# Kernel tuning notes

Hardware: AMD Instinct MI355X
Metric: run time of the kernel (lower is better)

Reference implementation:

```python
import jax, jax.numpy as jnp
import numpy as np

B, L, H, E, R = 2, 512, 768, 512, 32768
H2 = H // 2


def setup_inputs() -> dict:
    key = jax.random.key(0)
    ks = jax.random.split(key, 16)
    s = 0.02
    inp = {
        "hidden_states": jax.random.normal(ks[0], (B, L, H), dtype=jnp.float32),
        "ent_start": jax.random.randint(ks[1], (B, E), 0, L, dtype=jnp.int32),
        "ent_label": jax.random.randint(ks[2], (B, E), 0, 3, dtype=jnp.int32),
        "rel_head": jax.random.randint(ks[3], (B, R), 0, E, dtype=jnp.int32),
        "rel_tail": jax.random.randint(ks[4], (B, R), 0, E, dtype=jnp.int32),
        "rel_label": jax.random.randint(ks[5], (B, R), 0, 2, dtype=jnp.int32),
        "entity_emb": jax.random.normal(ks[6], (3, H), dtype=jnp.float32) * s,
        "head_W1": jax.random.normal(ks[7], (2 * H, H), dtype=jnp.float32) * s,
        "head_b1": jnp.zeros((H,), dtype=jnp.float32),
        "head_W2": jax.random.normal(ks[8], (H, H2), dtype=jnp.float32) * s,
        "head_b2": jnp.zeros((H2,), dtype=jnp.float32),
        "tail_W1": jax.random.normal(ks[9], (2 * H, H), dtype=jnp.float32) * s,
        "tail_b1": jnp.zeros((H,), dtype=jnp.float32),
        "tail_W2": jax.random.normal(ks[10], (H, H2), dtype=jnp.float32) * s,
        "tail_b2": jnp.zeros((H2,), dtype=jnp.float32),
        "bil_W": jax.random.normal(ks[11], (2, H2, H2), dtype=jnp.float32) * s,
        "lin_W": jax.random.normal(ks[12], (2 * H2, 2), dtype=jnp.float32) * s,
        "lin_b": jnp.zeros((2,), dtype=jnp.float32),
    }
    return inp


def _mlp(x, W1, b1, W2, b2):
    # Linear -> ReLU -> (dropout=identity) -> Linear -> ReLU -> (dropout=identity)
    h = jax.nn.relu(jnp.einsum("brd,dh->brh", x, W1) + b1)
    return jax.nn.relu(jnp.einsum("brh,hk->brk", h, W2) + b2)


def reference(hidden_states, ent_start, ent_label, rel_head, rel_tail, rel_label,
              entity_emb, head_W1, head_b1, head_W2, head_b2,
              tail_W1, tail_b1, tail_W2, tail_b2, bil_W, lin_W, lin_b):
    # Gather entity start token index and label for each relation endpoint
    h_idx = jnp.take_along_axis(ent_start, rel_head, axis=1)  # [B,R]
    t_idx = jnp.take_along_axis(ent_start, rel_tail, axis=1)
    h_lab = jnp.take_along_axis(ent_label, rel_head, axis=1)
    t_lab = jnp.take_along_axis(ent_label, rel_tail, axis=1)

    # Gather hidden states at entity start positions: [B,R,H]
    h_tok = jnp.take_along_axis(hidden_states, h_idx[..., None], axis=1)
    t_tok = jnp.take_along_axis(hidden_states, t_idx[..., None], axis=1)

    head_repr = jnp.concatenate([h_tok, entity_emb[h_lab]], axis=-1)  # [B,R,2H]
    tail_repr = jnp.concatenate([t_tok, entity_emb[t_lab]], axis=-1)

    heads = _mlp(head_repr, head_W1, head_b1, head_W2, head_b2)  # [B,R,H2]
    tails = _mlp(tail_repr, tail_W1, tail_b1, tail_W2, tail_b2)

    # BiaffineAttention: bilinear(x1,x2) + linear(cat(x1,x2))
    bil = jnp.einsum("brd,ode,bre->bro", heads, bil_W, tails)  # [B,R,2]
    lin = jnp.einsum("brc,co->bro", jnp.concatenate([heads, tails], axis=-1), lin_W) + lin_b
    logits = bil + lin  # [B,R,2]

    # Per-doc mean cross-entropy, summed over docs (matches loss accumulation)
    logp = jax.nn.log_softmax(logits, axis=-1)
    ce = -jnp.take_along_axis(logp, rel_label[..., None], axis=-1)[..., 0]  # [B,R]
    loss = ce.mean(axis=-1).sum()

    return loss, logits.reshape(B * R, 2)
```

## Files before the change

### kernel.cpp

```cpp
#include <hip/hip_runtime.h>
#include <math.h>

#define BB 2
#define LL 512
#define HH 768
#define EE 512
#define RR 32768
#define H2 384
#define MM 1024

typedef __attribute__((ext_vector_type(8))) short     bf16x8;
typedef __attribute__((ext_vector_type(4))) float     f32x4;
typedef __attribute__((ext_vector_type(8))) unsigned short u16x8;

__device__ __forceinline__ unsigned short f2bf(float f) {
    unsigned int u = __float_as_uint(f);
    u = (u + 0x7FFFu + ((u >> 16) & 1u)) >> 16;
    return (unsigned short)u;
}

__global__ __launch_bounds__(256) void prep(
    const float* __restrict__ hW1, const float* __restrict__ tW1,
    const float* __restrict__ hW2, const float* __restrict__ tW2,
    const float* __restrict__ bilW,
    unsigned short* __restrict__ W1ht, unsigned short* __restrict__ W1tt,
    unsigned short* __restrict__ W2ht, unsigned short* __restrict__ W2tt,
    unsigned short* __restrict__ bW0t, unsigned short* __restrict__ bW1t,
    const float* __restrict__ hidden, const int* __restrict__ ent_start,
    const int* __restrict__ ent_label, const float* __restrict__ emb,
    const float* __restrict__ hb1, const float* __restrict__ tb1,
    unsigned short* __restrict__ Hbf, float* __restrict__ embc,
    float* __restrict__ hlin, float* __restrict__ tlin, float* __restrict__ out)
{
    __shared__ unsigned short T[32 * 40];
    __shared__ float red[4][192];
    const int bid = blockIdx.x;
    const int t = threadIdx.x;

    if (bid == 3064) {
        const float4 z = {0.f, 0.f, 0.f, 0.f};
        ((float4*)hlin)[t] = z; ((float4*)hlin)[256 + t] = z;
        ((float4*)tlin)[t] = z; ((float4*)tlin)[256 + t] = z;
        if (t == 0) out[0] = 0.f;
        return;
    }

    if (bid >= 3040) {
        const int eb = bid - 3040;
        const int tc = t & 63;
        const int kg = t >> 6;
        const int n = eb * 64 + tc;
        const float* W = (n < 768) ? hW1 : tW1;
        const int cc = (n < 768) ? n : n - 768;
        float a0 = 0.f, a1 = 0.f, a2 = 0.f;
        const int kbeg = kg * 192;
        #pragma unroll 8
        for (int k = kbeg; k < kbeg + 192; ++k) {
            const float w = W[(size_t)(768 + k) * 768 + cc];
            a0 += emb[k] * w;
            a1 += emb[768 + k] * w;
            a2 += emb[1536 + k] * w;
        }
        red[kg][0 * 64 + tc] = a0;
        red[kg][1 * 64 + tc] = a1;
        red[kg][2 * 64 + tc] = a2;
        __syncthreads();
        if (kg == 0) {
            const float b = (n < 768) ? hb1[n] : tb1[n - 768];
            #pragma unroll
            for (int l = 0; l < 3; ++l) {
                embc[l * 1536 + n] = b + red[0][l * 64 + tc] + red[1][l * 64 + tc]
                                       + red[2][l * 64 + tc] + red[3][l * 64 + tc];
            }
        }
        return;
    }

    if (bid >= 2016) {
        const int m = bid - 2016;
        if (t >= 96) return;
        const int b = m >> 9;
        const int idx = ent_start[m];
        const float4* s = (const float4*)(hidden + (size_t)(b * LL + idx) * HH);
        const float4 v0 = s[2 * t];
        const float4 v1 = s[2 * t + 1];
        u16x8 o;
        o[0] = f2bf(v0.x); o[1] = f2bf(v0.y); o[2] = f2bf(v0.z); o[3] = f2bf(v0.w);
        o[4] = f2bf(v1.x); o[5] = f2bf(v1.y); o[6] = f2bf(v1.z); o[7] = f2bf(v1.w);
        *(u16x8*)(Hbf + (size_t)m * 768 + 8 * t) = o;
        return;
    }

    const float* src; unsigned short* dst; int K, N, tile;
    if (bid < 576)       { src = hW1;            dst = W1ht; K = 768; N = 768; tile = bid; }
    else if (bid < 1152) { src = tW1;            dst = W1tt; K = 768; N = 768; tile = bid - 576; }
    else if (bid < 1440) { src = hW2;            dst = W2ht; K = 768; N = 384; tile = bid - 1152; }
    else if (bid < 1728) { src = tW2;            dst = W2tt; K = 768; N = 384; tile = bid - 1440; }
    else if (bid < 1872) { src = bilW;           dst = bW0t; K = 384; N = 384; tile = bid - 1728; }
    else                 { src = bilW + 384*384; dst = bW1t; K = 384; N = 384; tile = bid - 1872; }
    const int tn = N >> 5;
    const int n0 = (tile % tn) * 32;
    const int k0 = (tile / tn) * 32;

    const int r  = t >> 3;
    const int c4 = (t & 7) * 4;
    const float4 g = *(const float4*)(src + (size_t)(k0 + r) * N + n0 + c4);
    T[(c4 + 0) * 40 + r] = f2bf(g.x);
    T[(c4 + 1) * 40 + r] = f2bf(g.y);
    T[(c4 + 2) * 40 + r] = f2bf(g.z);
    T[(c4 + 3) * 40 + r] = f2bf(g.w);
    __syncthreads();
    const int n  = t >> 3;
    const int k4 = (t & 7) * 4;
    *(ushort4*)(dst + (size_t)(n0 + n) * K + k0 + k4) = *(ushort4*)&T[n * 40 + k4];
}

template<bool RELU, bool BIAS, bool EB, bool WF32, bool WBF16, bool O2, bool LIN>
__global__ __launch_bounds__(256) void gemm_mfma(
    const unsigned short* __restrict__ A, int lda, int aoff1,
    const unsigned short* __restrict__ Bt0, const unsigned short* __restrict__ Bt1,
    int ldb, int bt_mrow, int Nh,
    const float* __restrict__ bias0, const float* __restrict__ bias1,
    const float* __restrict__ embc, const int* __restrict__ labels,
    const float* __restrict__ linW, float* __restrict__ hlin, float* __restrict__ tlin,
    int K, float* __restrict__ Cf, unsigned short* __restrict__ Cb, int ldc)
{
    __shared__ unsigned short As[2][64 * 72];
    __shared__ unsigned short Bs[2][64 * 72];

    const int tid = threadIdx.x;
    const int n0 = blockIdx.x * 64;
    const int m0 = blockIdx.y * 64;
    const int hf = (n0 >= Nh) ? 1 : 0;
    const unsigned short* Bt = hf ? Bt1 : Bt0;
    const int nc0 = n0 - (hf ? Nh : 0);
    const int aoff = hf ? aoff1 : 0;

    const int sr = tid >> 2;
    const int sk = (tid & 3) * 16;

    const unsigned short* Ap = A + (size_t)(m0 + sr) * lda + aoff + sk;
    const unsigned short* Bp = Bt + (size_t)((m0 >> 9) * bt_mrow + nc0 + sr) * ldb + sk;

    const int lane = tid & 63;
    const int wave = tid >> 6;
    const int wm = (wave & 1) * 32;
    const int wn = (wave >> 1) * 32;
    const int l15 = lane & 15;
    const int quad = lane >> 4;

    f32x4 acc00 = {}, acc01 = {}, acc10 = {}, acc11 = {};

    u16x8 a0v = *(const u16x8*)(Ap);
    u16x8 a1v = *(const u16x8*)(Ap + 8);
    u16x8 b0v = *(const u16x8*)(Bp);
    u16x8 b1v = *(const u16x8*)(Bp + 8);
    const int swo = sr * 72 + sk;
    *(u16x8*)&As[0][swo] = a0v; *(u16x8*)&As[0][swo + 8] = a1v;
    *(u16x8*)&Bs[0][swo] = b0v; *(u16x8*)&Bs[0][swo + 8] = b1v;

    const int NT = K >> 6;
    const int aro = quad * 8;
    int cur = 0;
    for (int it = 0; it < NT; ++it) {
        if (it + 1 < NT) {
            const int ko = (it + 1) * 64;
            a0v = *(const u16x8*)(Ap + ko); a1v = *(const u16x8*)(Ap + ko + 8);
            b0v = *(const u16x8*)(Bp + ko); b1v = *(const u16x8*)(Bp + ko + 8);
        }
        asm volatile("s_waitcnt lgkmcnt(0)" ::: "memory");
        __builtin_amdgcn_s_barrier();
        __builtin_amdgcn_sched_barrier(0);
        const unsigned short* Ac = As[cur];
        const unsigned short* Bc = Bs[cur];
        const bf16x8 fa0 = *(const bf16x8*)&Ac[(wm + l15) * 72 + aro];
        const bf16x8 fa1 = *(const bf16x8*)&Ac[(wm + 16 + l15) * 72 + aro];
        const bf16x8 fb0 = *(const bf16x8*)&Bc[(wn + l15) * 72 + aro];
        const bf16x8 fb1 = *(const bf16x8*)&Bc[(wn + 16 + l15) * 72 + aro];
        const bf16x8 ga0 = *(const bf16x8*)&Ac[(wm + l15) * 72 + aro + 32];
        const bf16x8 ga1 = *(const bf16x8*)&Ac[(wm + 16 + l15) * 72 + aro + 32];
        const bf16x8 gb0 = *(const bf16x8*)&Bc[(wn + l15) * 72 + aro + 32];
        const bf16x8 gb1 = *(const bf16x8*)&Bc[(wn + 16 + l15) * 72 + aro + 32];
        acc00 = __builtin_amdgcn_mfma_f32_16x16x32_bf16(fa0, fb0, acc00, 0, 0, 0);
        acc01 = __builtin_amdgcn_mfma_f32_16x16x32_bf16(fa0, fb1, acc01, 0, 0, 0);
        acc10 = __builtin_amdgcn_mfma_f32_16x16x32_bf16(fa1, fb0, acc10, 0, 0, 0);
        acc11 = __builtin_amdgcn_mfma_f32_16x16x32_bf16(fa1, fb1, acc11, 0, 0, 0);
        acc00 = __builtin_amdgcn_mfma_f32_16x16x32_bf16(ga0, gb0, acc00, 0, 0, 0);
        acc01 = __builtin_amdgcn_mfma_f32_16x16x32_bf16(ga0, gb1, acc01, 0, 0, 0);
        acc10 = __builtin_amdgcn_mfma_f32_16x16x32_bf16(ga1, gb0, acc10, 0, 0, 0);
        acc11 = __builtin_amdgcn_mfma_f32_16x16x32_bf16(ga1, gb1, acc11, 0, 0, 0);
        if (it + 1 < NT) {
            unsigned short* Aw = &As[cur ^ 1][0];
            unsigned short* Bw = &Bs[cur ^ 1][0];
            *(u16x8*)&Aw[swo] = a0v; *(u16x8*)&Aw[swo + 8] = a1v;
            *(u16x8*)&Bw[swo] = b0v; *(u16x8*)&Bw[swo + 8] = b1v;
        }
        cur ^= 1;
    }

    float bias_v0 = 0.f, bias_v1 = 0.f;
    if (BIAS) {
        const float* bb = hf ? bias1 : bias0;
        bias_v0 = bb[nc0 + wn + l15];
        bias_v1 = bb[nc0 + wn + 16 + l15];
    }
    const int col0 = n0 + wn + l15;
    const int col1 = col0 + 16;
    int colw0 = col0, colw1 = col1;
    if (O2) {
        colw0 = 2 * (nc0 + wn + l15) + hf;
        colw1 = 2 * (nc0 + wn + 16 + l15) + hf;
    }
    float2 lw0 = {0.f, 0.f}, lw1 = {0.f, 0.f};
    float* lout = nullptr;
    if (LIN) {
        lw0 = ((const float2*)linW)[col0];
        lw1 = ((const float2*)linW)[col1];
        lout = hf ? tlin : hlin;
    }
    const f32x4 accs[2][2] = {{acc00, acc01}, {acc10, acc11}};
    #pragma unroll
    for (int mi = 0; mi < 2; ++mi) {
        #pragma unroll
        for (int r = 0; r < 4; ++r) {
            const int row = m0 + wm + mi * 16 + quad * 4 + r;
            float v0 = accs[mi][0][r];
            float v1 = accs[mi][1][r];
            if (BIAS) { v0 += bias_v0; v1 += bias_v1; }
            if (EB) {
                const int lab = labels[row];
                v0 += embc[lab * 1536 + col0];
                v1 += embc[lab * 1536 + col1];
            }
            if (RELU) { v0 = fmaxf(v0, 0.f); v1 = fmaxf(v1, 0.f); }
            if (WF32) {
                Cf[(size_t)row * ldc + colw0] = v0;
                Cf[(size_t)row * ldc + colw1] = v1;
            }
            if (WBF16) {
                Cb[(size_t)row * ldc + colw0] = f2bf(v0);
                Cb[(size_t)row * ldc + colw1] = f2bf(v1);
            }
            if (LIN) {
                float s0 = v0 * lw0.x + v1 * lw1.x;
                float s1 = v0 * lw0.y + v1 * lw1.y;
                #pragma unroll
                for (int o = 8; o >= 1; o >>= 1) {
                    s0 += __shfl_xor(s0, o, 64);
                    s1 += __shfl_xor(s1, o, 64);
                }
                if (l15 == 0) {
                    atomicAdd(&lout[2 * row],     s0);
                    atomicAdd(&lout[2 * row + 1], s1);
                }
            }
        }
    }
}

__global__ __launch_bounds__(256) void rel_gather(
    const float* __restrict__ Stab,
    const float* __restrict__ hlin, const float* __restrict__ tlin,
    const float* __restrict__ lin_b,
    const int* __restrict__ rel_head, const int* __restrict__ rel_tail,
    const int* __restrict__ rel_label,
    float* __restrict__ out)
{
    const int tid = threadIdx.x;
    const int i = blockIdx.x * 256 + tid;
    const int b = i >> 15;
    const int h = rel_head[i];
    const int t = rel_tail[i];
    const int lab = rel_label[i];
    const int mh = (b << 9) + h;
    const int mt = (b << 9) + t;

    const float2 hl = ((const float2*)hlin)[mh];
    const float2 tl = ((const float2*)tlin)[mt];
    const float2 zz = *(const float2*)(Stab + (size_t)mh * 1024 + 2 * t);
    const float z0 = zz.x + hl.x + tl.x + lin_b[0];
    const float z1 = zz.y + hl.y + tl.y + lin_b[1];
    out[1 + 2 * (size_t)i]     = z0;
    out[2 + 2 * (size_t)i]     = z1;

    const float mx = fmaxf(z0, z1);
    const float mn = fminf(z0, z1);
    const float lse = mx + log1pf(expf(mn - mx));
    float ce = lse - (lab ? z1 : z0);

    #pragma unroll
    for (int o = 32; o >= 1; o >>= 1) ce += __shfl_xor(ce, o, 64);
    __shared__ float wsum[4];
    if ((tid & 63) == 0) wsum[tid >> 6] = ce;
    __syncthreads();
    if (tid == 0) {
        const float bs = wsum[0] + wsum[1] + wsum[2] + wsum[3];
        atomicAdd(out, bs * (1.0f / (float)RR));
    }
}

extern "C" void kernel_launch(void* const* d_in, const int* in_sizes, int n_in,
                              void* d_out, int out_size, void* d_ws, size_t ws_size,
                              hipStream_t stream) {
    const float* hidden    = (const float*)d_in[0];
    const int*   ent_start = (const int*)d_in[1];
    const int*   ent_label = (const int*)d_in[2];
    const int*   rel_head  = (const int*)d_in[3];
    const int*   rel_tail  = (const int*)d_in[4];
    const int*   rel_label = (const int*)d_in[5];
    const float* emb       = (const float*)d_in[6];
    const float* head_W1   = (const float*)d_in[7];
    const float* head_b1   = (const float*)d_in[8];
    const float* head_W2   = (const float*)d_in[9];
    const float* head_b2   = (const float*)d_in[10];
    const float* tail_W1   = (const float*)d_in[11];
    const float* tail_b1   = (const float*)d_in[12];
    const float* tail_W2   = (const float*)d_in[13];
    const float* tail_b2   = (const float*)d_in[14];
    const float* bil_W     = (const float*)d_in[15];
    const float* lin_W     = (const float*)d_in[16];
    const float* lin_b     = (const float*)d_in[17];
    float* out = (float*)d_out;

    char* w = (char*)d_ws;
    auto carve = [&](size_t bytes) {
        char* p = w; w += (bytes + 255) & ~(size_t)255; return p;
    };
    unsigned short* Hbf  = (unsigned short*)carve((size_t)MM * 768 * 2);
    unsigned short* Y1bf = (unsigned short*)carve((size_t)MM * 1536 * 2);
    unsigned short* HTbf = (unsigned short*)carve((size_t)MM * 768 * 2);
    unsigned short* hWbf = (unsigned short*)carve((size_t)MM * 768 * 2);
    float*          Stab = (float*)carve((size_t)MM * 1024 * 4);
    unsigned short* W1ht = (unsigned short*)carve((size_t)768 * 768 * 2);
    unsigned short* W1tt = (unsigned short*)carve((size_t)768 * 768 * 2);
    unsigned short* W2ht = (unsigned short*)carve((size_t)384 * 768 * 2);
    unsigned short* W2tt = (unsigned short*)carve((size_t)384 * 768 * 2);
    unsigned short* bW0t = (unsigned short*)carve((size_t)384 * 384 * 2);
    unsigned short* bW1t = (unsigned short*)carve((size_t)384 * 384 * 2);
    float*          embc = (float*)carve((size_t)3 * 1536 * 4);
    float*          hlin = (float*)carve(2048 * 4);
    float*          tlin = (float*)carve(2048 * 4);

    prep<<<3065, 256, 0, stream>>>(
        head_W1, tail_W1, head_W2, tail_W2, bil_W,
        W1ht, W1tt, W2ht, W2tt, bW0t, bW1t,
        hidden, ent_start, ent_label, emb, head_b1, tail_b1, Hbf, embc,
        hlin, tlin, out);

    gemm_mfma<true, false, true, false, true, false, false>
        <<<dim3(24, 16), 256, 0, stream>>>(
        Hbf, 768, 0, W1ht, W1tt, 768, 0, 768, nullptr, nullptr, embc, ent_label,
        nullptr, nullptr, nullptr, 768, nullptr, Y1bf, 1536);

    gemm_mfma<true, true, false, false, true, false, true>
        <<<dim3(12, 16), 256, 0, stream>>>(
        Y1bf, 1536, 768, W2ht, W2tt, 768, 0, 384, head_b2, tail_b2, nullptr, nullptr,
        lin_W, hlin, tlin, 768, nullptr, HTbf, 768);

    gemm_mfma<false, false, false, false, true, false, false>
        <<<dim3(12, 16), 256, 0, stream>>>(
        HTbf, 768, 0, bW0t, bW1t, 384, 0, 384, nullptr, nullptr, nullptr, nullptr,
        nullptr, nullptr, nullptr, 384, nullptr, hWbf, 768);

    gemm_mfma<false, false, false, true, false, true, false>
        <<<dim3(16, 16), 256, 0, stream>>>(
        hWbf, 768, 384, HTbf + 384, HTbf + 384, 768, 512, 512,
        nullptr, nullptr, nullptr, nullptr,
        nullptr, nullptr, nullptr, 384, Stab, nullptr, 1024);

    rel_gather<<<256, 256, 0, stream>>>(Stab, hlin, tlin, lin_b,
                                        rel_head, rel_tail, rel_label, out);
}
```

Measured before the change: 142.5 us.

## Overlap W2/bilinear weight transposes with first GEMM and deepen K-tile to 128

Transposing and converting the second-layer and bilinear weights moves out of the prep kernel into extra blocks of the first GEMM launch, so that work runs concurrently with the GEMM tiles and prep gets shorter. The GEMM body also doubles the K step per pipeline stage from 64 to 128. That halves the number of barrier-synchronized iterations but doubles shared memory per block, which may reduce occupancy. All GEMMs now share the refactored body.

```diff
diff --git a/kernel.cpp b/kernel.cpp
--- a/kernel.cpp
+++ b/kernel.cpp
@@ -13,21 +13,40 @@
 typedef __attribute__((ext_vector_type(4))) float     f32x4;
 typedef __attribute__((ext_vector_type(8))) unsigned short u16x8;
 
+#define BUFE (64 * 136)
+
 __device__ __forceinline__ unsigned short f2bf(float f) {
     unsigned int u = __float_as_uint(f);
     u = (u + 0x7FFFu + ((u >> 16) & 1u)) >> 16;
     return (unsigned short)u;
 }
 
+__device__ __forceinline__ void wtrans(const float* __restrict__ src,
+                                       unsigned short* __restrict__ dst,
+                                       int K, int N, int tile, unsigned short* T)
+{
+    const int t = threadIdx.x;
+    const int tn = N >> 5;
+    const int n0 = (tile % tn) * 32;
+    const int k0 = (tile / tn) * 32;
+    const int r  = t >> 3;
+    const int c4 = (t & 7) * 4;
+    const float4 g = *(const float4*)(src + (size_t)(k0 + r) * N + n0 + c4);
+    T[(c4 + 0) * 40 + r] = f2bf(g.x);
+    T[(c4 + 1) * 40 + r] = f2bf(g.y);
+    T[(c4 + 2) * 40 + r] = f2bf(g.z);
+    T[(c4 + 3) * 40 + r] = f2bf(g.w);
+    __syncthreads();
+    const int n  = t >> 3;
+    const int k4 = (t & 7) * 4;
+    *(ushort4*)(dst + (size_t)(n0 + n) * K + k0 + k4) = *(ushort4*)&T[n * 40 + k4];
+}
+
 __global__ __launch_bounds__(256) void prep(
     const float* __restrict__ hW1, const float* __restrict__ tW1,
-    const float* __restrict__ hW2, const float* __restrict__ tW2,
-    const float* __restrict__ bilW,
     unsigned short* __restrict__ W1ht, unsigned short* __restrict__ W1tt,
-    unsigned short* __restrict__ W2ht, unsigned short* __restrict__ W2tt,
-    unsigned short* __restrict__ bW0t, unsigned short* __restrict__ bW1t,
     const float* __restrict__ hidden, const int* __restrict__ ent_start,
-    const int* __restrict__ ent_label, const float* __restrict__ emb,
+    const float* __restrict__ emb,
     const float* __restrict__ hb1, const float* __restrict__ tb1,
     unsigned short* __restrict__ Hbf, float* __restrict__ embc,
     float* __restrict__ hlin, float* __restrict__ tlin, float* __restrict__ out)
@@ -37,7 +56,7 @@
     const int bid = blockIdx.x;
     const int t = threadIdx.x;
 
-    if (bid == 3064) {
+    if (bid == 2200) {
         const float4 z = {0.f, 0.f, 0.f, 0.f};
         ((float4*)hlin)[t] = z; ((float4*)hlin)[256 + t] = z;
         ((float4*)tlin)[t] = z; ((float4*)tlin)[256 + t] = z;
@@ -45,8 +64,8 @@
         return;
     }
 
-    if (bid >= 3040) {
-        const int eb = bid - 3040;
+    if (bid >= 2176) {
+        const int eb = bid - 2176;
         const int tc = t & 63;
         const int kg = t >> 6;
         const int n = eb * 64 + tc;
@@ -76,8 +95,8 @@
         return;
     }
 
-    if (bid >= 2016) {
-        const int m = bid - 2016;
+    if (bid >= 1152) {
+        const int m = bid - 1152;
         if (t >= 96) return;
         const int b = m >> 9;
         const int idx = ent_start[m];
@@ -91,53 +110,32 @@
         return;
     }
 
-    const float* src; unsigned short* dst; int K, N, tile;
-    if (bid < 576)       { src = hW1;            dst = W1ht; K = 768; N = 768; tile = bid; }
-    else if (bid < 1152) { src = tW1;            dst = W1tt; K = 768; N = 768; tile = bid - 576; }
-    else if (bid < 1440) { src = hW2;            dst = W2ht; K = 768; N = 384; tile = bid - 1152; }
-    else if (bid < 1728) { src = tW2;            dst = W2tt; K = 768; N = 384; tile = bid - 1440; }
-    else if (bid < 1872) { src = bilW;           dst = bW0t; K = 384; N = 384; tile = bid - 1728; }
-    else                 { src = bilW + 384*384; dst = bW1t; K = 384; N = 384; tile = bid - 1872; }
-    const int tn = N >> 5;
-    const int n0 = (tile % tn) * 32;
-    const int k0 = (tile / tn) * 32;
-
-    const int r  = t >> 3;
-    const int c4 = (t & 7) * 4;
-    const float4 g = *(const float4*)(src + (size_t)(k0 + r) * N + n0 + c4);
-    T[(c4 + 0) * 40 + r] = f2bf(g.x);
-    T[(c4 + 1) * 40 + r] = f2bf(g.y);
-    T[(c4 + 2) * 40 + r] = f2bf(g.z);
-    T[(c4 + 3) * 40 + r] = f2bf(g.w);
-    __syncthreads();
-    const int n  = t >> 3;
-    const int k4 = (t & 7) * 4;
-    *(ushort4*)(dst + (size_t)(n0 + n) * K + k0 + k4) = *(ushort4*)&T[n * 40 + k4];
+    if (bid < 576) wtrans(hW1, W1ht, 768, 768, bid, T);
+    else           wtrans(tW1, W1tt, 768, 768, bid - 576, T);
 }
 
 template<bool RELU, bool BIAS, bool EB, bool WF32, bool WBF16, bool O2, bool LIN>
-__global__ __launch_bounds__(256) void gemm_mfma(
+__device__ __forceinline__ void gemm_body(
+    int tile, int nx,
     const unsigned short* __restrict__ A, int lda, int aoff1,
     const unsigned short* __restrict__ Bt0, const unsigned short* __restrict__ Bt1,
     int ldb, int bt_mrow, int Nh,
     const float* __restrict__ bias0, const float* __restrict__ bias1,
     const float* __restrict__ embc, const int* __restrict__ labels,
     const float* __restrict__ linW, float* __restrict__ hlin, float* __restrict__ tlin,
-    int K, float* __restrict__ Cf, unsigned short* __restrict__ Cb, int ldc)
-{
-    __shared__ unsigned short As[2][64 * 72];
-    __shared__ unsigned short Bs[2][64 * 72];
-
+    int K, float* __restrict__ Cf, unsigned short* __restrict__ Cb, int ldc,
+    unsigned short* As, unsigned short* Bs)
+{
     const int tid = threadIdx.x;
-    const int n0 = blockIdx.x * 64;
-    const int m0 = blockIdx.y * 64;
+    const int n0 = (tile % nx) * 64;
+    const int m0 = (tile / nx) * 64;
     const int hf = (n0 >= Nh) ? 1 : 0;
     const unsigned short* Bt = hf ? Bt1 : Bt0;
     const int nc0 = n0 - (hf ? Nh : 0);
     const int aoff = hf ? aoff1 : 0;
 
     const int sr = tid >> 2;
-    const int sk = (tid & 3) * 16;
+    const int sk = (tid & 3) * 32;
 
     const unsigned short* Ap = A + (size_t)(m0 + sr) * lda + aoff + sk;
     const unsigned short* Bp = Bt + (size_t)((m0 >> 9) * bt_mrow + nc0 + sr) * ldb + sk;
@@ -151,49 +149,51 @@
 
     f32x4 acc00 = {}, acc01 = {}, acc10 = {}, acc11 = {};
 
-    u16x8 a0v = *(const u16x8*)(Ap);
-    u16x8 a1v = *(const u16x8*)(Ap + 8);
-    u16x8 b0v = *(const u16x8*)(Bp);
-    u16x8 b1v = *(const u16x8*)(Bp + 8);
-    const int swo = sr * 72 + sk;
-    *(u16x8*)&As[0][swo] = a0v; *(u16x8*)&As[0][swo + 8] = a1v;
-    *(u16x8*)&Bs[0][swo] = b0v; *(u16x8*)&Bs[0][swo + 8] = b1v;
-
-    const int NT = K >> 6;
+    u16x8 av0 = *(const u16x8*)(Ap);      u16x8 av1 = *(const u16x8*)(Ap + 8);
+    u16x8 av2 = *(const u16x8*)(Ap + 16); u16x8 av3 = *(const u16x8*)(Ap + 24);
+    u16x8 bv0 = *(const u16x8*)(Bp);      u16x8 bv1 = *(const u16x8*)(Bp + 8);
+    u16x8 bv2 = *(const u16x8*)(Bp + 16); u16x8 bv3 = *(const u16x8*)(Bp + 24);
+    const int swo = sr * 136 + sk;
+    *(u16x8*)&As[swo] = av0;      *(u16x8*)&As[swo + 8] = av1;
+    *(u16x8*)&As[swo + 16] = av2; *(u16x8*)&As[swo + 24] = av3;
+    *(u16x8*)&Bs[swo] = bv0;      *(u16x8*)&Bs[swo + 8] = bv1;
+    *(u16x8*)&Bs[swo + 16] = bv2; *(u16x8*)&Bs[swo + 24] = bv3;
+
+    const int NT = K >> 7;
     const int aro = quad * 8;
     int cur = 0;
     for (int it = 0; it < NT; ++it) {
         if (it + 1 < NT) {
-            const int ko = (it + 1) * 64;
-            a0v = *(const u16x8*)(Ap + ko); a1v = *(const u16x8*)(Ap + ko + 8);
-            b0v = *(const u16x8*)(Bp + ko); b1v = *(const u16x8*)(Bp + ko + 8);
+            const int ko = (it + 1) * 128;
+            av0 = *(const u16x8*)(Ap + ko);      av1 = *(const u16x8*)(Ap + ko + 8);
+            av2 = *(const u16x8*)(Ap + ko + 16); av3 = *(const u16x8*)(Ap + ko + 24);
+            bv0 = *(const u16x8*)(Bp + ko);      bv1 = *(const u16x8*)(Bp + ko + 8);
+            bv2 = *(const u16x8*)(Bp + ko + 16); bv3 = *(const u16x8*)(Bp + ko + 24);
         }
         asm volatile("s_waitcnt lgkmcnt(0)" ::: "memory");
         __builtin_amdgcn_s_barrier();
         __builtin_amdgcn_sched_barrier(0);
-        const unsigned short* Ac = As[cur];
-        const unsigned short* Bc = Bs[cur];
-        const bf16x8 fa0 = *(const bf16x8*)&Ac[(wm + l15) * 72 + aro];
-        const bf16x8 fa1 = *(const bf16x8*)&Ac[(wm + 16 + l15) * 72 + aro];
-        const bf16x8 fb0 = *(const bf16x8*)&Bc[(wn + l15) * 72 + aro];
-        const bf16x8 fb1 = *(const bf16x8*)&Bc[(wn + 16 + l15) * 72 + aro];
-        const bf16x8 ga0 = *(const bf16x8*)&Ac[(wm + l15) * 72 + aro + 32];
-        const bf16x8 ga1 = *(const bf16x8*)&Ac[(wm + 16 + l15) * 72 + aro + 32];
-        const bf16x8 gb0 = *(const bf16x8*)&Bc[(wn + l15) * 72 + aro + 32];
-        const bf16x8 gb1 = *(const bf16x8*)&Bc[(wn + 16 + l15) * 72 + aro + 32];
-        acc00 = __builtin_amdgcn_mfma_f32_16x16x32_bf16(fa0, fb0, acc00, 0, 0, 0);
-        acc01 = __builtin_amdgcn_mfma_f32_16x16x32_bf16(fa0, fb1, acc01, 0, 0, 0);
-        acc10 = __builtin_amdgcn_mfma_f32_16x16x32_bf16(fa1, fb0, acc10, 0, 0, 0);
-        acc11 = __builtin_amdgcn_mfma_f32_16x16x32_bf16(fa1, fb1, acc11, 0, 0, 0);
-        acc00 = __builtin_amdgcn_mfma_f32_16x16x32_bf16(ga0, gb0, acc00, 0, 0, 0);
-        acc01 = __builtin_amdgcn_mfma_f32_16x16x32_bf16(ga0, gb1, acc01, 0, 0, 0);
-        acc10 = __builtin_amdgcn_mfma_f32_16x16x32_bf16(ga1, gb0, acc10, 0, 0, 0);
-        acc11 = __builtin_amdgcn_mfma_f32_16x16x32_bf16(ga1, gb1, acc11, 0, 0, 0);
+        const unsigned short* Ac = As + cur * BUFE;
+        const unsigned short* Bc = Bs + cur * BUFE;
+        #pragma unroll
+        for (int s = 0; s < 4; ++s) {
+            const int ks = s * 32 + aro;
+            const bf16x8 fa0 = *(const bf16x8*)&Ac[(wm + l15) * 136 + ks];
+            const bf16x8 fa1 = *(const bf16x8*)&Ac[(wm + 16 + l15) * 136 + ks];
+            const bf16x8 fb0 = *(const bf16x8*)&Bc[(wn + l15) * 136 + ks];
+            const bf16x8 fb1 = *(const bf16x8*)&Bc[(wn + 16 + l15) * 136 + ks];
+            acc00 = __builtin_amdgcn_mfma_f32_16x16x32_bf16(fa0, fb0, acc00, 0, 0, 0);
+            acc01 = __builtin_amdgcn_mfma_f32_16x16x32_bf16(fa0, fb1, acc01, 0, 0, 0);
+            acc10 = __builtin_amdgcn_mfma_f32_16x16x32_bf16(fa1, fb0, acc10, 0, 0, 0);
+            acc11 = __builtin_amdgcn_mfma_f32_16x16x32_bf16(fa1, fb1, acc11, 0, 0, 0);
+        }
         if (it + 1 < NT) {
-            unsigned short* Aw = &As[cur ^ 1][0];
-            unsigned short* Bw = &Bs[cur ^ 1][0];
-            *(u16x8*)&Aw[swo] = a0v; *(u16x8*)&Aw[swo + 8] = a1v;
-            *(u16x8*)&Bw[swo] = b0v; *(u16x8*)&Bw[swo + 8] = b1v;
+            unsigned short* Aw = As + (cur ^ 1) * BUFE;
+            unsigned short* Bw = Bs + (cur ^ 1) * BUFE;
+            *(u16x8*)&Aw[swo] = av0;      *(u16x8*)&Aw[swo + 8] = av1;
+            *(u16x8*)&Aw[swo + 16] = av2; *(u16x8*)&Aw[swo + 24] = av3;
+            *(u16x8*)&Bw[swo] = bv0;      *(u16x8*)&Bw[swo + 8] = bv1;
+            *(u16x8*)&Bw[swo + 16] = bv2; *(u16x8*)&Bw[swo + 24] = bv3;
         }
         cur ^= 1;
     }
@@ -258,6 +258,52 @@
     }
 }
 
+template<bool RELU, bool BIAS, bool EB, bool WF32, bool WBF16, bool O2, bool LIN>
+__global__ __launch_bounds__(256) void gemm_mfma(
+    const unsigned short* __restrict__ A, int lda, int aoff1,
+    const unsigned short* __restrict__ Bt0, const unsigned short* __restrict__ Bt1,
+    int ldb, int bt_mrow, int Nh,
+    const float* __restrict__ bias0, const float* __restrict__ bias1,
+    const float* __restrict__ embc, const int* __restrict__ labels,
+    const float* __restrict__ linW, float* __restrict__ hlin, float* __restrict__ tlin,
+    int K, float* __restrict__ Cf, unsigned short* __restrict__ Cb, int ldc)
+{
+    __shared__ __align__(16) unsigned short As[2 * BUFE];
+    __shared__ __align__(16) unsigned short Bs[2 * BUFE];
+    gemm_body<RELU, BIAS, EB, WF32, WBF16, O2, LIN>(
+        blockIdx.y * gridDim.x + blockIdx.x, gridDim.x,
+        A, lda, aoff1, Bt0, Bt1, ldb, bt_mrow, Nh,
+        bias0, bias1, embc, labels, linW, hlin, tlin,
+        K, Cf, Cb, ldc, As, Bs);
+}
+
+__global__ __launch_bounds__(256) void gemm1_plus(
+    const unsigned short* __restrict__ Hbf,
+    const unsigned short* __restrict__ W1ht, const unsigned short* __restrict__ W1tt,
+    const float* __restrict__ embc, const int* __restrict__ ent_label,
+    unsigned short* __restrict__ Y1bf,
+    const float* __restrict__ hW2, const float* __restrict__ tW2,
+    const float* __restrict__ bilW,
+    unsigned short* __restrict__ W2ht, unsigned short* __restrict__ W2tt,
+    unsigned short* __restrict__ bW0t, unsigned short* __restrict__ bW1t)
+{
+    __shared__ __align__(16) unsigned short As[2 * BUFE];
+    __shared__ __align__(16) unsigned short Bs[2 * BUFE];
+    const int bid = blockIdx.x;
+    if (bid >= 384) {
+        const int task = bid - 384;
+        if (task < 288)      wtrans(hW2, W2ht, 768, 384, task, As);
+        else if (task < 576) wtrans(tW2, W2tt, 768, 384, task - 288, As);
+        else if (task < 720) wtrans(bilW, bW0t, 384, 384, task - 576, As);
+        else                 wtrans(bilW + 384 * 384, bW1t, 384, 384, task - 720, As);
+        return;
+    }
+    gemm_body<true, false, true, false, true, false, false>(
+        bid, 24, Hbf, 768, 0, W1ht, W1tt, 768, 0, 768,
+        nullptr, nullptr, embc, ent_label, nullptr, nullptr, nullptr,
+        768, nullptr, Y1bf, 1536, As, Bs);
+}
+
 __global__ __launch_bounds__(256) void rel_gather(
     const float* __restrict__ Stab,
     const float* __restrict__ hlin, const float* __restrict__ tlin,
@@ -280,8 +326,8 @@
     const float2 zz = *(const float2*)(Stab + (size_t)mh * 1024 + 2 * t);
     const float z0 = zz.x + hl.x + tl.x + lin_b[0];
     const float z1 = zz.y + hl.y + tl.y + lin_b[1];
-    out[1 + 2 * (size_t)i]     = z0;
-    out[2 + 2 * (size_t)i]     = z1;
+    out[1 + 2 * (size_t)i] = z0;
+    out[2 + 2 * (size_t)i] = z1;
 
     const float mx = fmaxf(z0, z1);
     const float mn = fminf(z0, z1);
@@ -341,32 +387,30 @@
     float*          hlin = (float*)carve(2048 * 4);
     float*          tlin = (float*)carve(2048 * 4);
 
-    prep<<<3065, 256, 0, stream>>>(
-        head_W1, tail_W1, head_W2, tail_W2, bil_W,
-        W1ht, W1tt, W2ht, W2tt, bW0t, bW1t,
-        hidden, ent_start, ent_label, emb, head_b1, tail_b1, Hbf, embc,
+    prep<<<2201, 256, 0, stream>>>(
+        head_W1, tail_W1, W1ht, W1tt,
+        hidden, ent_start, emb, head_b1, tail_b1, Hbf, embc,
         hlin, tlin, out);
 
-    gemm_mfma<true, false, true, false, true, false, false>
-        <<<dim3(24, 16), 256, 0, stream>>>(
-        Hbf, 768, 0, W1ht, W1tt, 768, 0, 768, nullptr, nullptr, embc, ent_label,
-        nullptr, nullptr, nullptr, 768, nullptr, Y1bf, 1536);
+    gemm1_plus<<<1248, 256, 0, stream>>>(
+        Hbf, W1ht, W1tt, embc, ent_label, Y1bf,
+        head_W2, tail_W2, bil_W, W2ht, W2tt, bW0t, bW1t);
 
     gemm_mfma<true, true, false, false, true, false, true>
         <<<dim3(12, 16), 256, 0, stream>>>(
-        Y1bf, 1536, 768, W2ht, W2tt, 768, 0, 384, head_b2, tail_b2, nullptr, nullptr,
-        lin_W, hlin, tlin, 768, nullptr, HTbf, 768);
+        Y1bf, 1536, 768, W2ht, W2tt, 768, 0, 384, head_b2, tail_b2,
+        nullptr, nullptr, lin_W, hlin, tlin, 768, nullptr, HTbf, 768);
 
     gemm_mfma<false, false, false, false, true, false, false>
         <<<dim3(12, 16), 256, 0, stream>>>(
-        HTbf, 768, 0, bW0t, bW1t, 384, 0, 384, nullptr, nullptr, nullptr, nullptr,
-        nullptr, nullptr, nullptr, 384, nullptr, hWbf, 768);
+        HTbf, 768, 0, bW0t, bW1t, 384, 0, 384, nullptr, nullptr,
+        nullptr, nullptr, nullptr, nullptr, nullptr, 384, nullptr, hWbf, 768);
 
     gemm_mfma<false, false, false, true, false, true, false>
         <<<dim3(16, 16), 256, 0, stream>>>(
         hWbf, 768, 384, HTbf + 384, HTbf + 384, 768, 512, 512,
-        nullptr, nullptr, nullptr, nullptr,
-        nullptr, nullptr, nullptr, 384, Stab, nullptr, 1024);
+        nullptr, nullptr, nullptr, nullptr, nullptr, nullptr, nullptr,
+        384, Stab, nullptr, 1024);
 
     rel_gather<<<256, 256, 0, stream>>>(Stab, hlin, tlin, lin_b,
                                         rel_head, rel_tail, rel_label, out);
```

Measured after the change: 147.4 us. +3.5%, slower.
